# Kernel optimization log

Measured on AMD Instinct MI355X. Metric: run time of the kernel, lower is better.

The kernel has to match this reference:

```python
import jax, jax.numpy as jnp
import numpy as np
import math

GAMMA = 2.0
ALPHA = 0.25
SIZES = [[64, 64], [32, 32], [16, 16], [8, 8], [4, 4]]
RATIOS = [0.5, 1.0, 2.0]
SCALES = [1.0, 2.0 ** (1.0 / 3.0), 2.0 ** (2.0 / 3.0)]
B, T, C = 16, 64, 80


def _create_anchors(sizes, ratios, scales):
    # replicates torch create_anchors (cthw format, normalized [-1,1] coords)
    aspects = np.array([[[s * math.sqrt(r), s * math.sqrt(1.0 / r)] for s in scales]
                        for r in ratios], dtype=np.float64).reshape(-1, 2)
    out = []
    for (h, w) in sizes:
        sized = 4.0 * (aspects * np.array([2.0 / h, 2.0 / w]))  # [a,2]
        rows = np.linspace(-1 + 1.0 / h, 1 - 1.0 / h, h) if h > 1 else np.array([0.0])
        cols = np.linspace(-1 + 1.0 / w, 1 - 1.0 / w, w) if w > 1 else np.array([0.0])
        gy, gx = np.meshgrid(rows, cols, indexing='ij')
        grid = np.stack([gy, gx], -1).reshape(-1, 1, 2)  # [h*w,1,2]
        n, a = grid.shape[0], aspects.shape[0]
        anc = np.concatenate([np.broadcast_to(grid, (n, a, 2)),
                              np.broadcast_to(sized[None], (n, a, 2))], 2)
        out.append(anc.reshape(-1, 4))
    return jnp.asarray(np.concatenate(out, 0), dtype=jnp.float32)


def _cthw2tlbr(b):
    return jnp.concatenate([b[..., :2] - b[..., 2:] / 2, b[..., :2] + b[..., 2:] / 2], -1)


def _tlbr2cthw(b):
    return jnp.concatenate([(b[..., :2] + b[..., 2:]) / 2, b[..., 2:] - b[..., :2]], -1)


def _iou(anchors, tgts):
    # anchors [A,4] cthw, tgts [T,4] cthw -> [A,T]
    a_t, t_t = _cthw2tlbr(anchors), _cthw2tlbr(tgts)
    tl = jnp.maximum(a_t[:, None, :2], t_t[None, :, :2])
    br = jnp.minimum(a_t[:, None, 2:], t_t[None, :, 2:])
    sz = jnp.clip(br - tl, 0.0)
    inter = sz[..., 0] * sz[..., 1]
    a_sz = anchors[:, 2] * anchors[:, 3]
    t_sz = tgts[:, 2] * tgts[:, 3]
    union = a_sz[:, None] + t_sz[None, :] - inter
    return inter / (union + 1e-8)


def _bbox_to_activ(bboxes, anchors):
    tc = (bboxes[..., :2] - anchors[..., :2]) / anchors[..., 2:]
    ts = jnp.log(bboxes[..., 2:] / anchors[..., 2:] + 1e-8)
    return jnp.concatenate([tc, ts], -1) / jnp.array([0.1, 0.1, 0.2, 0.2], dtype=bboxes.dtype)


def _one_loss(clas_pred, bbox_pred, clas_tgt, bbox_tgt_tlbr, anchors):
    Tn = clas_tgt.shape[0]
    tgt = _tlbr2cthw(bbox_tgt_tlbr)
    valid = clas_tgt > 0                       # pad_idx = 0 -> padded targets invalid
    iou = jnp.where(valid[None, :], _iou(anchors, tgt), -1.0)  # [A,T]
    vals = iou.max(axis=1)
    idxs = iou.argmax(axis=1)
    # -1 background, -2 ignore band (0.4 <= iou <= 0.5)
    matches = jnp.where(vals > 0.5, idxs, jnp.where(vals < 0.4, -1, -2))
    pos = matches >= 0
    safe = jnp.clip(matches, 0, Tn - 1)
    # smooth_l1 (beta=1, mean over selected elements)
    reg_tgt = _bbox_to_activ(tgt[safe], anchors)
    d = bbox_pred - reg_tgt
    ad = jnp.abs(d)
    sl1 = jnp.where(ad < 1.0, 0.5 * d * d, ad - 0.5)
    npos = pos.sum().astype(clas_pred.dtype)
    bb_loss = (sl1 * pos[:, None]).sum() / jnp.maximum(4.0 * npos, 1.0)
    # class targets: matched anchors get 1-based class, background -> 0
    cls = jnp.where(pos, clas_tgt[safe], 0)
    clas_mask = matches >= -1                  # exclude ignored anchors
    enc = jax.nn.one_hot(cls - 1, clas_pred.shape[1], dtype=clas_pred.dtype)  # cls=0 -> all-zero row
    ps = jax.nn.sigmoid(clas_pred)
    w = (enc * (1 - ps) + (1 - enc) * ps) ** GAMMA * ((1 - enc) * ALPHA + enc * (1 - ALPHA))
    w = jax.lax.stop_gradient(w)               # weights.detach() in torch
    bce = -(enc * jax.nn.log_sigmoid(clas_pred) + (1 - enc) * jax.nn.log_sigmoid(-clas_pred))
    clas_loss = (w * bce * clas_mask[:, None].astype(clas_pred.dtype)).sum()
    return bb_loss + clas_loss / jnp.maximum(npos, 1.0)


def setup_inputs() -> dict:
    key = jax.random.key(0)
    k1, k2, k3, k4, k5 = jax.random.split(key, 5)
    anchors = _create_anchors(SIZES, RATIOS, SCALES)
    A = anchors.shape[0]
    clas_preds = jax.random.normal(k1, (B, A, C), dtype=jnp.float32)
    bbox_preds = jax.random.normal(k2, (B, A, 4), dtype=jnp.float32) * 0.1
    centers = jax.random.uniform(k3, (B, T, 2), minval=-0.7, maxval=0.7)
    sizes = jax.random.uniform(k4, (B, T, 2), minval=0.05, maxval=0.5)
    bbox_tgts = jnp.concatenate([centers - sizes / 2, centers + sizes / 2], -1)  # tlbr
    clas_tgts = jax.random.randint(k5, (B, T), 1, C + 1)  # 1-based labels, no padding
    return {"clas_preds": clas_preds, "bbox_preds": bbox_preds,
            "bbox_tgts": bbox_tgts, "clas_tgts": clas_tgts, "anchors": anchors}


def reference(clas_preds, bbox_preds, bbox_tgts, clas_tgts, anchors):
    per_img = jax.vmap(_one_loss, in_axes=(0, 0, 0, 0, None))(
        clas_preds, bbox_preds, clas_tgts, bbox_tgts, anchors)
    return per_img.sum() / clas_preds.shape[0]
```

## Files before the change

### kernel.cpp

```cpp
#include <hip/hip_runtime.h>
#include <cstdint>
#include <cstddef>

#define TPB 256
#define MAXT 128

#define K_BG 0.17328679514f

__device__ __forceinline__ float f_bg4(float4 v) {
    float r = 0.f;
    const float xs[4] = {v.x, v.y, v.z, v.w};
    #pragma unroll
    for (int i = 0; i < 4; ++i) {
        const float x  = xs[i];
        const float u  = x * 1.44269504089f;
        const float em = __builtin_amdgcn_exp2f(-fabsf(u));
        const float oe = 1.f + em;
        const float l2 = __builtin_amdgcn_logf(oe);
        const float s  = __builtin_amdgcn_rcpf(oe);
        const float sp2 = fmaxf(u, 0.f) + l2;
        const float p  = (x >= 0.f) ? s : (1.f - s);
        r = fmaf(p * p, sp2, r);
    }
    return r;
}

__device__ __forceinline__ float f_fg_minus_bg(float x) {
    const float ax = fabsf(x);
    const float em = __builtin_amdgcn_exp2f(ax * -1.44269504089f);
    const float oe = 1.f + em;
    const float l  = __builtin_amdgcn_logf(oe) * 0.69314718056f;
    const float s  = __builtin_amdgcn_rcpf(oe);
    const float sp_p = (x >= 0.f) ? (x + l) : l;
    const float sp_n = sp_p - x;
    const float p  = (x >= 0.f) ? s : (1.f - s);
    const float q  = 1.f - p;
    return 0.75f * q * q * sp_n - 0.25f * p * p * sp_p;
}

template<int C4T>
__global__ __launch_bounds__(TPB, 4)
void fused_kernel(const float* __restrict__ bbox_preds,
                  const float* __restrict__ bbox_tgts,
                  const int*   __restrict__ clas_tgts,
                  const float* __restrict__ anchors,
                  const float* __restrict__ clas_preds,
                  int A, int T, int C4rt,
                  float* __restrict__ np_p,
                  float* __restrict__ bb_p,
                  float* __restrict__ cl_p,
                  int nblk)
{
    const int C4  = (C4T > 0) ? C4T : C4rt;
    const int b   = blockIdx.y;
    const int a0  = blockIdx.x * TPB;
    const int tid = threadIdx.x;
    const int a   = a0 + tid;
    const bool in = (a < A);

    __shared__ float4 s_ta[MAXT];
    __shared__ float4 s_tb[MAXT];
    __shared__ float2 s_tc[MAXT];
    for (int i = tid; i < T; i += TPB) {
        const float4 tg = reinterpret_cast<const float4*>(bbox_tgts)[(size_t)b * T + i];
        const int   cl = clas_tgts[(size_t)b * T + i];
        const float c0 = (tg.x + tg.z) * 0.5f, c1 = (tg.y + tg.w) * 0.5f;
        const float s0 = tg.z - tg.x,          s1 = tg.w - tg.y;
        const bool  val = (cl > 0);
        s_ta[i] = val ? make_float4(c0 - s0 * 0.5f, c1 - s1 * 0.5f,
                                    c0 + s0 * 0.5f, c1 + s1 * 0.5f)
                      : make_float4(1e30f, 1e30f, -1e30f, -1e30f);
        s_tb[i] = make_float4(c0, c1, s0, s1);
        s_tc[i] = make_float2(val ? s0 * s1 : 0.f, (float)cl);
    }

    float4 anc = make_float4(0.f, 0.f, 1.f, 1.f);
    if (in) anc = reinterpret_cast<const float4*>(anchors)[a];
    const float a_tl0 = anc.x - anc.z * 0.5f;
    const float a_tl1 = anc.y - anc.w * 0.5f;
    const float a_br0 = anc.x + anc.z * 0.5f;
    const float a_br1 = anc.y + anc.w * 0.5f;
    const float a_area = anc.z * anc.w;

    __syncthreads();

    const int nA = min(TPB, A - a0);
    const float4* tile = reinterpret_cast<const float4*>(clas_preds)
                         + ((size_t)b * A + a0) * C4;

    float raw  = 0.f;
    float best = -1e30f;
    int   besti = 0;

#define IOU_STEP(t)                                                         \
    {                                                                       \
        const float4 ta = s_ta[t];                                          \
        const float2 tc = s_tc[t];                                          \
        const float tl0 = fmaxf(a_tl0, ta.x);                               \
        const float tl1 = fmaxf(a_tl1, ta.y);                               \
        const float br0 = fminf(a_br0, ta.z);                               \
        const float br1 = fminf(a_br1, ta.w);                               \
        const float sz0 = fmaxf(br0 - tl0, 0.0f);                           \
        const float sz1 = fmaxf(br1 - tl1, 0.0f);                           \
        const float inter = sz0 * sz1;                                      \
        const float uni = a_area + tc.x - inter;                            \
        const float iou = inter * __builtin_amdgcn_rcpf(uni + 1e-8f);       \
        if (iou > best) { best = iou; besti = (t); }                        \
    }

    if (C4T > 0 && nA == TPB) {
        constexpr int CH  = 5;
        constexpr int NCH = (C4T > 0 ? C4T : 5) / CH;
        const int TCH = T / NCH;
        float4 cur[CH];
        #pragma unroll
        for (int i = 0; i < CH; ++i) cur[i] = tile[tid + i * TPB];
        #pragma unroll
        for (int g = 0; g < NCH; ++g) {
            float4 nxt[CH];
            if (g + 1 < NCH) {
                #pragma unroll
                for (int i = 0; i < CH; ++i)
                    nxt[i] = tile[tid + ((g + 1) * CH + i) * TPB];
            }
            #pragma unroll
            for (int i = 0; i < CH; ++i) raw += f_bg4(cur[i]);
            const int t0 = g * TCH;
            #pragma unroll 4
            for (int t = t0; t < t0 + TCH; ++t) IOU_STEP(t)
            if (g + 1 < NCH) {
                #pragma unroll
                for (int i = 0; i < CH; ++i) cur[i] = nxt[i];
            }
        }
        for (int t = (T / NCH) * NCH; t < T; ++t) IOU_STEP(t)
    } else {
        const int tot = nA * C4;
        for (int j = tid; j < tot; j += TPB)
            raw += f_bg4(tile[j]);
        #pragma unroll 4
        for (int t = 0; t < T; ++t) IOU_STEP(t)
    }
#undef IOU_STEP

    const bool pos = in && (best > 0.5f);
    const bool ign = in && !pos && !(best < 0.4f);

    float sl1 = 0.f;
    int   cls = 0;
    if (pos) {
        const float4 tb  = s_tb[besti];
        cls = (int)s_tc[besti].y;
        const float4 bp = reinterpret_cast<const float4*>(bbox_preds)[(size_t)b * A + a];
        const float tc0 = (tb.x - anc.x) / anc.z;
        const float tc1 = (tb.y - anc.y) / anc.w;
        const float ts0 = logf(tb.z / anc.z + 1e-8f);
        const float ts1 = logf(tb.w / anc.w + 1e-8f);
        const float r0 = tc0 / 0.1f, r1 = tc1 / 0.1f;
        const float r2 = ts0 / 0.2f, r3 = ts1 / 0.2f;
        const float d0 = bp.x - r0, d1 = bp.y - r1, d2 = bp.z - r2, d3 = bp.w - r3;
        const float a0f = fabsf(d0), a1f = fabsf(d1), a2f = fabsf(d2), a3f = fabsf(d3);
        sl1 += (a0f < 1.f) ? 0.5f * d0 * d0 : a0f - 0.5f;
        sl1 += (a1f < 1.f) ? 0.5f * d1 * d1 : a1f - 0.5f;
        sl1 += (a2f < 1.f) ? 0.5f * d2 * d2 : a2f - 0.5f;
        sl1 += (a3f < 1.f) ? 0.5f * d3 * d3 : a3f - 0.5f;
    }

    const int lane = tid & 63;
    const int wid  = tid >> 6;
    const unsigned long long pball = __ballot(pos);
    const unsigned long long iball = __ballot(ign);

    __shared__ int s_pc[TPB / 64], s_ic[TPB / 64];
    __shared__ int s_plist[TPB], s_pcls[TPB], s_ilist[TPB];
    if (lane == 0) { s_pc[wid] = __popcll(pball); s_ic[wid] = __popcll(iball); }
    __syncthreads();
    int p_off = 0, i_off = 0, p_total = 0, i_total = 0;
    #pragma unroll
    for (int w = 0; w < TPB / 64; ++w) {
        if (w < wid) { p_off += s_pc[w]; i_off += s_ic[w]; }
        p_total += s_pc[w]; i_total += s_ic[w];
    }
    const unsigned long long lmask = (lane == 63) ? ~0ULL >> 1 : (1ULL << lane) - 1;
    if (pos) {
        const int idx = p_off + __popcll(pball & lmask);
        s_plist[idx] = a; s_pcls[idx] = cls;
    }
    if (ign) {
        const int idx = i_off + __popcll(iball & lmask);
        s_ilist[idx] = a;
    }
    __syncthreads();

    float corr = 0.f;
    if (tid < p_total) {
        const int pa = s_plist[tid];
        const int pc = s_pcls[tid];
        const float x = clas_preds[((size_t)b * A + pa) * (C4 * 4) + (pc - 1)];
        corr += f_fg_minus_bg(x);
    }
    const int ig_elems = i_total * C4;
    for (int j = tid; j < ig_elems; j += TPB) {
        const int ii = j / C4;
        const int c4 = j - ii * C4;
        const int ia = s_ilist[ii];
        raw -= f_bg4(reinterpret_cast<const float4*>(clas_preds)
                         [((size_t)b * A + ia) * C4 + c4]);
    }

    float v = sl1;
    float u = fmaf(raw, K_BG, corr);
    #pragma unroll
    for (int off = 32; off; off >>= 1) {
        v += __shfl_down(v, off);
        u += __shfl_down(u, off);
    }
    __shared__ float s_sl1[TPB / 64], s_cl[TPB / 64];
    if (lane == 0) { s_sl1[wid] = v; s_cl[wid] = u; }
    __syncthreads();
    if (tid == 0) {
        float tv = 0.f, tu = 0.f;
        #pragma unroll
        for (int w = 0; w < TPB / 64; ++w) { tv += s_sl1[w]; tu += s_cl[w]; }
        const size_t o = (size_t)b * nblk + blockIdx.x;
        bb_p[o] = tv;
        cl_p[o] = tu;
        np_p[o] = (float)p_total;
    }
}

__global__ void reduce_kernel(const float* __restrict__ np_p,
                              const float* __restrict__ bb_p,
                              const float* __restrict__ cl_p,
                              int nblk, int Bn,
                              float* __restrict__ out)
{
    const int wid  = threadIdx.x >> 6;
    const int lane = threadIdx.x & 63;
    const int nw   = blockDim.x >> 6;
    __shared__ float s_loss[32];

    float acc = 0.f;
    for (int b = wid; b < Bn; b += nw) {
        float cl = 0.f, bb = 0.f, np = 0.f;
        for (int i = lane; i < nblk; i += 64) {
            const size_t o = (size_t)b * nblk + i;
            np += np_p[o]; bb += bb_p[o]; cl += cl_p[o];
        }
        #pragma unroll
        for (int off = 32; off; off >>= 1) {
            cl += __shfl_down(cl, off);
            bb += __shfl_down(bb, off);
            np += __shfl_down(np, off);
        }
        if (lane == 0)
            acc += bb / fmaxf(4.f * np, 1.f) + cl / fmaxf(np, 1.f);
    }
    if (lane == 0) s_loss[wid] = acc;
    __syncthreads();
    if (threadIdx.x == 0) {
        float v = 0.f;
        for (int w = 0; w < nw; ++w) v += s_loss[w];
        out[0] = v / (float)Bn;
    }
}

extern "C" void kernel_launch(void* const* d_in, const int* in_sizes, int n_in,
                              void* d_out, int out_size, void* d_ws, size_t ws_size,
                              hipStream_t stream)
{
    const float* clas_preds = (const float*)d_in[0];
    const float* bbox_preds = (const float*)d_in[1];
    const float* bbox_tgts  = (const float*)d_in[2];
    const int*   clas_tgts  = (const int*)d_in[3];
    const float* anchors    = (const float*)d_in[4];

    const int A  = in_sizes[4] / 4;
    const int Bn = in_sizes[1] / (A * 4);
    const int T  = in_sizes[3] / Bn;
    const int C  = in_sizes[0] / (Bn * A);
    const int C4 = C / 4;

    const int nblk = (A + TPB - 1) / TPB;

    char* ws = (char*)d_ws;
    float* np_p = (float*)ws;  ws += (size_t)Bn * nblk * sizeof(float);
    float* bb_p = (float*)ws;  ws += (size_t)Bn * nblk * sizeof(float);
    float* cl_p = (float*)ws;

    dim3 g1((unsigned)nblk, (unsigned)Bn);
    if (C4 == 20) {
        fused_kernel<20><<<g1, TPB, 0, stream>>>(
            bbox_preds, bbox_tgts, clas_tgts, anchors, clas_preds,
            A, T, C4, np_p, bb_p, cl_p, nblk);
    } else {
        fused_kernel<0><<<g1, TPB, 0, stream>>>(
            bbox_preds, bbox_tgts, clas_tgts, anchors, clas_preds,
            A, T, C4, np_p, bb_p, cl_p, nblk);
    }

    reduce_kernel<<<1, 1024, 0, stream>>>(np_p, bb_p, cl_p, nblk, Bn, (float*)d_out);
}
```

Measured before the change: 65.23 us.

## Cull targets per block by anchor bounding box and compare IoU division-free

Each block reduces the bounding box of its 256 anchors and builds a compacted list of targets that can overlap it, so the IoU loop only visits targets that may intersect. IoU comparisons are done by cross-multiplying intersection and union instead of taking a reciprocal, and the first class-prediction loads are issued before the target setup to overlap latency. This adds two wave reductions, an extra barrier and indirect shared-memory indexing, and replaces the unrolled fixed-trip IoU loop with a variable-length one.

```diff
diff --git a/kernel.cpp b/kernel.cpp
--- a/kernel.cpp
+++ b/kernel.cpp
@@ -4,6 +4,7 @@
 
 #define TPB 256
 #define MAXT 128
+#define BIGC 1e18f
 
 #define K_BG 0.17328679514f
 
@@ -57,10 +58,24 @@
     const int tid = threadIdx.x;
     const int a   = a0 + tid;
     const bool in = (a < A);
+    const int lane = tid & 63;
+    const int wid  = tid >> 6;
+
+    const int nA = min(TPB, A - a0);
+    const float4* tile = reinterpret_cast<const float4*>(clas_preds)
+                         + ((size_t)b * A + a0) * C4;
+
+    constexpr int CH  = 5;
+    constexpr int NCH = (C4T > 0 ? C4T : 5) / CH;
+    float4 cur[CH];
+    if (C4T > 0 && nA == TPB) {
+        #pragma unroll
+        for (int i = 0; i < CH; ++i) cur[i] = tile[tid + i * TPB];
+    }
 
     __shared__ float4 s_ta[MAXT];
     __shared__ float4 s_tb[MAXT];
-    __shared__ float2 s_tc[MAXT];
+    __shared__ int    s_cls[MAXT];
     for (int i = tid; i < T; i += TPB) {
         const float4 tg = reinterpret_cast<const float4*>(bbox_tgts)[(size_t)b * T + i];
         const int   cl = clas_tgts[(size_t)b * T + i];
@@ -69,9 +84,9 @@
         const bool  val = (cl > 0);
         s_ta[i] = val ? make_float4(c0 - s0 * 0.5f, c1 - s1 * 0.5f,
                                     c0 + s0 * 0.5f, c1 + s1 * 0.5f)
-                      : make_float4(1e30f, 1e30f, -1e30f, -1e30f);
+                      : make_float4(BIGC, BIGC, BIGC, BIGC);
         s_tb[i] = make_float4(c0, c1, s0, s1);
-        s_tc[i] = make_float2(val ? s0 * s1 : 0.f, (float)cl);
+        s_cls[i] = cl;
     }
 
     float4 anc = make_float4(0.f, 0.f, 1.f, 1.f);
@@ -80,22 +95,60 @@
     const float a_tl1 = anc.y - anc.w * 0.5f;
     const float a_br0 = anc.x + anc.z * 0.5f;
     const float a_br1 = anc.y + anc.w * 0.5f;
-    const float a_area = anc.z * anc.w;
-
-    __syncthreads();
-
-    const int nA = min(TPB, A - a0);
-    const float4* tile = reinterpret_cast<const float4*>(clas_preds)
-                         + ((size_t)b * A + a0) * C4;
-
-    float raw  = 0.f;
-    float best = -1e30f;
+    const float a_area_eps = anc.z * anc.w + 1e-8f;
+
+    float m0 = in ? a_tl0 :  1e30f, m1 = in ? a_tl1 :  1e30f;
+    float M0 = in ? a_br0 : -1e30f, M1 = in ? a_br1 : -1e30f;
+    #pragma unroll
+    for (int off = 32; off; off >>= 1) {
+        m0 = fminf(m0, __shfl_down(m0, off));
+        m1 = fminf(m1, __shfl_down(m1, off));
+        M0 = fmaxf(M0, __shfl_down(M0, off));
+        M1 = fmaxf(M1, __shfl_down(M1, off));
+    }
+    __shared__ float s_red[4][TPB / 64];
+    if (lane == 0) {
+        s_red[0][wid] = m0; s_red[1][wid] = m1;
+        s_red[2][wid] = M0; s_red[3][wid] = M1;
+    }
+    __syncthreads();
+
+    __shared__ int s_act[MAXT];
+    __shared__ int s_nact;
+    if (wid == 0) {
+        float bm0 = s_red[0][0], bm1 = s_red[1][0];
+        float bM0 = s_red[2][0], bM1 = s_red[3][0];
+        #pragma unroll
+        for (int w = 1; w < TPB / 64; ++w) {
+            bm0 = fminf(bm0, s_red[0][w]); bm1 = fminf(bm1, s_red[1][w]);
+            bM0 = fmaxf(bM0, s_red[2][w]); bM1 = fmaxf(bM1, s_red[3][w]);
+        }
+        bool act = false;
+        if (lane < T && T <= 64) {
+            const float4 ta = s_ta[lane];
+            act = (ta.x <= bM0) && (ta.y <= bM1) && (ta.z >= bm0) && (ta.w >= bm1);
+        }
+        const unsigned long long ball = __ballot(act);
+        if (act) {
+            const unsigned long long lm =
+                (lane == 63) ? ~0ULL >> 1 : (1ULL << lane) - 1;
+            s_act[__popcll(ball & lm)] = lane;
+        }
+        if (lane == 0) s_nact = __popcll(ball);
+    }
+    if (T > 64) {
+        for (int i = tid; i < T; i += TPB) s_act[i] = i;
+        if (tid == 0) s_nact = T;
+    }
+    __syncthreads();
+
+    const int nact = s_nact;
+    float bI = -1.f, bU = 1.f;
     int   besti = 0;
 
-#define IOU_STEP(t)                                                         \
+#define IOU_STEP(tt)                                                        \
     {                                                                       \
-        const float4 ta = s_ta[t];                                          \
-        const float2 tc = s_tc[t];                                          \
+        const float4 ta = s_ta[tt];                                         \
         const float tl0 = fmaxf(a_tl0, ta.x);                               \
         const float tl1 = fmaxf(a_tl1, ta.y);                               \
         const float br0 = fminf(a_br0, ta.z);                               \
@@ -103,18 +156,17 @@
         const float sz0 = fmaxf(br0 - tl0, 0.0f);                           \
         const float sz1 = fmaxf(br1 - tl1, 0.0f);                           \
         const float inter = sz0 * sz1;                                      \
-        const float uni = a_area + tc.x - inter;                            \
-        const float iou = inter * __builtin_amdgcn_rcpf(uni + 1e-8f);       \
-        if (iou > best) { best = iou; besti = (t); }                        \
-    }
-
+        const float tarea = (ta.z - ta.x) * (ta.w - ta.y);                  \
+        const float uni = a_area_eps + tarea - inter;                       \
+        const bool upd = inter * bU > bI * uni;       \
+        bI = upd ? inter : bI;                                              \
+        bU = upd ? uni   : bU;                                              \
+        besti = upd ? (tt) : besti;                                         \
+    }
+
+    float raw = 0.f;
     if (C4T > 0 && nA == TPB) {
-        constexpr int CH  = 5;
-        constexpr int NCH = (C4T > 0 ? C4T : 5) / CH;
-        const int TCH = T / NCH;
-        float4 cur[CH];
-        #pragma unroll
-        for (int i = 0; i < CH; ++i) cur[i] = tile[tid + i * TPB];
+        const int cs = (nact + NCH - 1) / NCH;
         #pragma unroll
         for (int g = 0; g < NCH; ++g) {
             float4 nxt[CH];
@@ -125,32 +177,29 @@
             }
             #pragma unroll
             for (int i = 0; i < CH; ++i) raw += f_bg4(cur[i]);
-            const int t0 = g * TCH;
-            #pragma unroll 4
-            for (int t = t0; t < t0 + TCH; ++t) IOU_STEP(t)
+            const int te = min((g + 1) * cs, nact);
+            for (int t = g * cs; t < te; ++t) IOU_STEP(s_act[t])
             if (g + 1 < NCH) {
                 #pragma unroll
                 for (int i = 0; i < CH; ++i) cur[i] = nxt[i];
             }
         }
-        for (int t = (T / NCH) * NCH; t < T; ++t) IOU_STEP(t)
     } else {
         const int tot = nA * C4;
         for (int j = tid; j < tot; j += TPB)
             raw += f_bg4(tile[j]);
-        #pragma unroll 4
-        for (int t = 0; t < T; ++t) IOU_STEP(t)
+        for (int t = 0; t < nact; ++t) IOU_STEP(s_act[t])
     }
 #undef IOU_STEP
 
-    const bool pos = in && (best > 0.5f);
-    const bool ign = in && !pos && !(best < 0.4f);
+    const bool pos = in && (bI > 0.5f * bU);
+    const bool ign = in && !pos && !(bI < 0.4f * bU);
 
     float sl1 = 0.f;
     int   cls = 0;
     if (pos) {
-        const float4 tb  = s_tb[besti];
-        cls = (int)s_tc[besti].y;
+        const float4 tb = s_tb[besti];
+        cls = s_cls[besti];
         const float4 bp = reinterpret_cast<const float4*>(bbox_preds)[(size_t)b * A + a];
         const float tc0 = (tb.x - anc.x) / anc.z;
         const float tc1 = (tb.y - anc.y) / anc.w;
@@ -166,8 +215,6 @@
         sl1 += (a3f < 1.f) ? 0.5f * d3 * d3 : a3f - 0.5f;
     }
 
-    const int lane = tid & 63;
-    const int wid  = tid >> 6;
     const unsigned long long pball = __ballot(pos);
     const unsigned long long iball = __ballot(ign);
 
```

Result: faster. 62.17 us (median of 2 runs) (-4.7%).
